# Kernel optimization log

Measured on AMD Instinct MI355X. Metric: run time of the kernel, lower is better.

Reference implementation:

```python
import jax, jax.numpy as jnp
import numpy as np

B, N, DIN, D, PHI, RHO, L = 4096, 10, 32, 128, 256, 128, 3
EPS = 1e-5


def setup_inputs() -> dict:
    key = jax.random.key(0)
    ks = jax.random.split(key, 24)
    def p(k, shape):
        return jax.random.normal(k, shape, jnp.float32) * 0.05
    return {
        "A": jax.random.normal(ks[0], (B, N, N), jnp.float32),
        "X": jax.random.normal(ks[1], (B, N, DIN), jnp.float32),
        "home_mask": jax.random.randint(ks[2], (B, N), 0, 2).astype(jnp.int32),
        "We1": p(ks[3], (DIN, D)), "be1": p(ks[4], (D,)),
        "We2": p(ks[5], (D, D)), "be2": p(ks[6], (D,)),
        "rgcn_w": p(ks[7], (L, 2, D, D)),      # per-relation weights
        "rgcn_root": p(ks[8], (L, D, D)),       # root (self) weight
        "rgcn_b": p(ks[9], (L, D)),
        "l1w": p(ks[10], (L, D, D)), "l1b": p(ks[11], (L, D)),
        "l2w": p(ks[12], (L, D, D)), "l2b": p(ks[13], (L, D)),
        "ln_g": jnp.ones((D,), jnp.float32), "ln_b": jnp.zeros((D,), jnp.float32),
        "p1w": p(ks[14], (D, PHI)), "p1b": p(ks[15], (PHI,)),
        "p2w": p(ks[16], (PHI, PHI)), "p2b": p(ks[17], (PHI,)),
        "r1w": p(ks[18], (PHI, RHO)), "r1b": p(ks[19], (RHO,)),
        "r2w": p(ks[20], (RHO, 1)), "r2b": p(ks[21], (1,)),
    }


def _layernorm(x, g, b):
    mu = x.mean(-1, keepdims=True)
    var = ((x - mu) ** 2).mean(-1, keepdims=True)
    return (x - mu) / jnp.sqrt(var + EPS) * g + b


def reference(A, X, home_mask, We1, be1, We2, be2, rgcn_w, rgcn_root, rgcn_b,
              l1w, l1b, l2w, l2b, ln_g, ln_b, p1w, p1b, p2w, p2b,
              r1w, r1b, r2w, r2b):
    BN = B * N
    hm = home_mask.astype(jnp.float32)
    am = 1.0 - hm
    # embedders (dropout layers are identity in eval)
    H = jax.nn.relu(X @ We1 + be1)
    H = (H @ We2 + be2).reshape(BN, D)
    # A ~ randn is nonzero everywhere -> edge list = all (b,i,j) pairs,
    # in the same row-major order torch.nonzero produces.
    bidx = jnp.repeat(jnp.arange(BN), N)          # b*N+i for each edge (row)
    row = bidx
    col = (jnp.repeat(jnp.arange(B), N * N) * N + jnp.tile(jnp.arange(N), BN))
    ew = A.reshape(-1)                             # edge weight
    aw = jnp.abs(ew)
    m1 = (ew > 0).astype(jnp.float32)              # relation 1 mask
    m0 = 1.0 - m1                                  # relation 0 mask
    agg = jnp.zeros_like(H)
    for l in range(L):
        H = H + agg
        # RGCNConv (mean aggregation per relation + root + bias)
        xj = H[row]                                # [E, D] gather of sources
        s0 = jax.ops.segment_sum(xj * m0[:, None], col, num_segments=BN)
        s1 = jax.ops.segment_sum(xj * m1[:, None], col, num_segments=BN)
        c0 = jax.ops.segment_sum(m0, col, num_segments=BN)
        c1 = jax.ops.segment_sum(m1, col, num_segments=BN)
        mean0 = s0 / jnp.maximum(c0, 1.0)[:, None]
        mean1 = s1 / jnp.maximum(c1, 1.0)[:, None]
        H2 = mean0 @ rgcn_w[l, 0] + mean1 @ rgcn_w[l, 1] + H @ rgcn_root[l] + rgcn_b[l]
        # outer gather-scale-scatter
        msg = H2[col] * aw[:, None]                # [E, D]
        agg = jax.ops.segment_sum(msg, row, num_segments=BN)
        agg = jax.nn.relu(_layernorm(agg, ln_g, ln_b))
        # Linear -> ReLU -> (Dropout=id) -> Linear
        agg = jax.nn.relu(agg @ l1w[l] + l1b[l])
        agg = agg @ l2w[l] + l2b[l]
    H = (H + agg).reshape(B, N, D)
    # DeepSet phi (dropout = identity)
    phi = jax.nn.relu(H @ p1w + p1b)
    phi = jax.nn.relu(phi @ p2w + p2b)             # [B, N, PHI]
    hs = (phi * hm[..., None]).sum(axis=1)
    aws = (phi * am[..., None]).sum(axis=1)
    def rho(s):
        return (jax.nn.relu(s @ r1w + r1b) @ r2w + r2b)[..., 0]
    return 0.5 + 0.5 * jnp.tanh(rho(hs) - rho(aws))
```

## Files before the change

### kernel.cpp

```cpp
#include <hip/hip_runtime.h>
#include <math.h>

#define B_    4096
#define N_    10
#define DIN_  32
#define D_    128
#define PHI_  256
#define RHO_  128
#define L_    3
#define EPS_  1e-5f

__device__ __forceinline__ short f2hs(float f) {
    union { _Float16 h; short s; } u;
    u.h = (_Float16)f;
    return u.s;
}
__device__ __forceinline__ float hs2f(short s) {
    union { _Float16 h; short s; } u;
    u.s = s;
    return (float)u.h;
}

typedef short    s16x8 __attribute__((ext_vector_type(8)));
typedef _Float16 h16x8 __attribute__((ext_vector_type(8)));
typedef float    f32x4 __attribute__((ext_vector_type(4)));
typedef float    v2f   __attribute__((ext_vector_type(2)));

__device__ __forceinline__ h16x8 ld8h(const short* p) {
    union { s16x8 s; h16x8 h; } u;
    u.s = *(const s16x8*)p;
    return u.h;
}
__device__ __forceinline__ h16x8 cvt8(const float* p) {
    f32x4 x0 = *(const f32x4*)p;
    f32x4 x1 = *(const f32x4*)(p + 4);
    h16x8 a;
    a[0]=(_Float16)x0[0]; a[1]=(_Float16)x0[1]; a[2]=(_Float16)x0[2]; a[3]=(_Float16)x0[3];
    a[4]=(_Float16)x1[0]; a[5]=(_Float16)x1[1]; a[6]=(_Float16)x1[2]; a[7]=(_Float16)x1[3];
    return a;
}

__device__ __forceinline__ v2f splat2(float s) { v2f r; r.x = s; r.y = s; return r; }
__device__ __forceinline__ v2f fma2(v2f a, v2f b, v2f c) { return __builtin_elementwise_fma(a, b, c); }

#define WS_WE1 0
#define WS_WE2 4096
#define WS_RGW 20480
#define WS_RGR 118784
#define WS_L1  167936
#define WS_L2  217088
#define WS_P1  266240
#define WS_P2  299008
#define WS_R1  364544

__global__ __launch_bounds__(256)
void prep_weights(const float* __restrict__ We1, const float* __restrict__ We2,
                  const float* __restrict__ rgw, const float* __restrict__ rgr,
                  const float* __restrict__ l1w, const float* __restrict__ l2w,
                  const float* __restrict__ p1w, const float* __restrict__ p2w,
                  const float* __restrict__ r1w, short* __restrict__ ws)
{
    int bi = blockIdx.x * 4 + (threadIdx.x >> 6);
    int l  = threadIdx.x & 63;
    const float* src; int KS, Nw, dstOff, tt;
    if      (bi <   8) { src = We1; KS = 1; Nw = 128; dstOff = WS_WE1; tt = bi; }
    else if (bi <  40) { src = We2; KS = 4; Nw = 128; dstOff = WS_WE2; tt = bi - 8; }
    else if (bi < 232) { int m = (bi - 40) >> 5;  src = rgw + m * 16384; KS = 4; Nw = 128; dstOff = WS_RGW + m * 16384; tt = (bi - 40)  & 31; }
    else if (bi < 328) { int m = (bi - 232) >> 5; src = rgr + m * 16384; KS = 4; Nw = 128; dstOff = WS_RGR + m * 16384; tt = (bi - 232) & 31; }
    else if (bi < 424) { int m = (bi - 328) >> 5; src = l1w + m * 16384; KS = 4; Nw = 128; dstOff = WS_L1  + m * 16384; tt = (bi - 328) & 31; }
    else if (bi < 520) { int m = (bi - 424) >> 5; src = l2w + m * 16384; KS = 4; Nw = 128; dstOff = WS_L2  + m * 16384; tt = (bi - 424) & 31; }
    else if (bi < 584) { src = p1w; KS = 4; Nw = 256; dstOff = WS_P1; tt = bi - 520; }
    else if (bi < 712) { src = p2w; KS = 8; Nw = 256; dstOff = WS_P2; tt = bi - 584; }
    else               { src = r1w; KS = 8; Nw = 128; dstOff = WS_R1; tt = bi - 712; }
    int nt = tt / KS, ks = tt - nt * KS;
    int kbase = ks * 32 + (l >> 4) * 8;
    int col   = nt * 16 + (l & 15);
    union { short s[8]; int4 v; } u;
#pragma unroll
    for (int j = 0; j < 8; ++j)
        u.s[j] = f2hs(src[(size_t)(kbase + j) * Nw + col]);
    *(int4*)(ws + dstOff + ((size_t)tt * 64 + l) * 8) = u.v;
}


#define MFMA16(a, b, c) __builtin_amdgcn_mfma_f32_16x16x32_f16(a, b, c, 0, 0, 0)

struct A4 { f32x4 p, q, r, s; };

__device__ __forceinline__ A4 a4init(const float* __restrict__ bias, int c16) {
    float b0 = bias[c16], b1 = bias[16 + c16];
    A4 c;
    c.p = (f32x4){b0, b0, b0, b0};
    c.q = (f32x4){b1, b1, b1, b1};
    c.r = c.p;
    c.s = c.q;
    return c;
}
__device__ __forceinline__ A4 a4zero() {
    A4 c;
    c.p = (f32x4){0.f, 0.f, 0.f, 0.f};
    c.q = c.p; c.r = c.p; c.s = c.p;
    return c;
}

template<int KS>
__device__ __forceinline__ A4 mm2q_a16(const short* __restrict__ Wf,
                                       const short* __restrict__ A0, const short* __restrict__ A1,
                                       int ldA, int mrow, int q, int l, A4 c) {
    static_assert(KS % 4 == 0, "KS must be a multiple of 4");
    const short* ap0 = A0 + mrow * ldA + q * 8;
    const short* ap1 = A1 + mrow * ldA + q * 8;
    const short* wp  = Wf + (size_t)l * 8;
#pragma unroll
    for (int kc = 0; kc < KS; kc += 4) {
        h16x8 fa0[4], fa1[4], fb0[4], fb1[4];
#pragma unroll
        for (int k = 0; k < 4; ++k) {
            fa0[k] = ld8h(ap0 + (kc + k) * 32);
            fa1[k] = ld8h(ap1 + (kc + k) * 32);
            fb0[k] = ld8h(wp + (size_t)(kc + k) * 512);
            fb1[k] = ld8h(wp + (size_t)(KS + kc + k) * 512);
        }
#pragma unroll
        for (int k = 0; k < 4; ++k) {
            c.p = MFMA16(fa0[k], fb0[k], c.p);
            c.r = MFMA16(fa1[k], fb0[k], c.r);
            c.q = MFMA16(fa0[k], fb1[k], c.q);
            c.s = MFMA16(fa1[k], fb1[k], c.s);
        }
    }
    return c;
}

template<int KS>
__device__ __forceinline__ A4 mm2q_a32(const short* __restrict__ Wf,
                                       const float* __restrict__ A0, const float* __restrict__ A1,
                                       int ldA, int mrow, int q, int l, A4 c) {
    static_assert(KS % 4 == 0, "KS must be a multiple of 4");
    const float* ap0 = A0 + mrow * ldA + q * 8;
    const float* ap1 = A1 + mrow * ldA + q * 8;
    const short* wp  = Wf + (size_t)l * 8;
#pragma unroll
    for (int kc = 0; kc < KS; kc += 4) {
        h16x8 fa0[4], fa1[4], fb0[4], fb1[4];
#pragma unroll
        for (int k = 0; k < 4; ++k) {
            fa0[k] = cvt8(ap0 + (kc + k) * 32);
            fa1[k] = cvt8(ap1 + (kc + k) * 32);
            fb0[k] = ld8h(wp + (size_t)(kc + k) * 512);
            fb1[k] = ld8h(wp + (size_t)(KS + kc + k) * 512);
        }
#pragma unroll
        for (int k = 0; k < 4; ++k) {
            c.p = MFMA16(fa0[k], fb0[k], c.p);
            c.r = MFMA16(fa1[k], fb0[k], c.r);
            c.q = MFMA16(fa0[k], fb1[k], c.q);
            c.s = MFMA16(fa1[k], fb1[k], c.s);
        }
    }
    return c;
}

#define HLD 132
#define SLD 392

template<bool RELU>
__device__ __forceinline__ void st2(f32x4 u, f32x4 v, short* __restrict__ dst, int q, int c16) {
#pragma unroll
    for (int i = 0; i < 4; ++i) {
        int r = q * 4 + i;
        if (r < 10) {
            float a = u[i], b = v[i];
            if (RELU) { a = fmaxf(a, 0.f); b = fmaxf(b, 0.f); }
            dst[r * SLD + c16]      = f2hs(a);
            dst[r * SLD + 16 + c16] = f2hs(b);
        }
    }
}

__device__ __forceinline__ void colsum1(f32x4 v4, const float* __restrict__ hmf,
                                        const float* __restrict__ awf,
                                        short* __restrict__ rho, int tt, int q, int c16, int l) {
    float v0 = fmaxf(v4[0], 0.f), v1 = fmaxf(v4[1], 0.f);
    float v2 = fmaxf(v4[2], 0.f), v3 = fmaxf(v4[3], 0.f);
    float hp = hmf[q * 4 + 0] * v0 + hmf[q * 4 + 1] * v1 + hmf[q * 4 + 2] * v2 + hmf[q * 4 + 3] * v3;
    float ap = awf[q * 4 + 0] * v0 + awf[q * 4 + 1] * v1 + awf[q * 4 + 2] * v2 + awf[q * 4 + 3] * v3;
    hp += __shfl_xor(hp, 16); hp += __shfl_xor(hp, 32);
    ap += __shfl_xor(ap, 16); ap += __shfl_xor(ap, 32);
    if (l < 16) {
        rho[tt * 16 + l]       = f2hs(hp);
        rho[256 + tt * 16 + l] = f2hs(ap);
    }
}

__device__ __forceinline__ void rhoepi1(f32x4 t0, f32x4 t1, const float* __restrict__ r2w,
                                        int wv, int q, int c16, int l, float* __restrict__ dSg) {
    float d = 0.f;
    if (q == 0) {
        d = (fmaxf(t0[0], 0.f) - fmaxf(t0[1], 0.f)) * r2w[(wv * 2 + 0) * 16 + c16];
        d = fmaf(fmaxf(t1[0], 0.f) - fmaxf(t1[1], 0.f), r2w[(wv * 2 + 1) * 16 + c16], d);
    }
#pragma unroll
    for (int off = 32; off > 0; off >>= 1) d += __shfl_xor(d, off);
    if (l == 0) dSg[wv] = d;
}

__global__ __attribute__((amdgpu_waves_per_eu(2, 5))) __launch_bounds__(256)
void gcn_main(const float* __restrict__ A, const float* __restrict__ X,
              const int* __restrict__ home_mask,
              const float* __restrict__ be1, const float* __restrict__ be2,
              const float* __restrict__ rgcn_b,
              const float* __restrict__ l1b, const float* __restrict__ l2b,
              const float* __restrict__ ln_g, const float* __restrict__ ln_b,
              const float* __restrict__ p1b, const float* __restrict__ p2b,
              const float* __restrict__ r1b, const float* __restrict__ r2w,
              const short* __restrict__ ws, float* __restrict__ out)
{
    const int b   = blockIdx.x;
    const int tid = threadIdx.x;
    const int wv  = tid >> 6;
    const int l   = tid & 63;
    const int q   = l >> 4;
    const int c16 = l & 15;
    const int mrow = (c16 < 10) ? c16 : 9;

    __shared__ __align__(16) float HfS[2][N_ * HLD];
    __shared__ __align__(16) short StS[2][N_ * SLD];
    __shared__ __align__(16) short RhoS[2][512];
    __shared__ float AsS[2][100];
    __shared__ float C0S[2][100], C1S[2][100];
    __shared__ float invc0S[2][N_], invc1S[2][N_], rsAS[2][N_];
    __shared__ float hmfS[2][16], awfS[2][16];
    __shared__ float dS[8];

    if (tid < 200) {
        int g = tid / 100, e = tid - g * 100;
        AsS[g][e] = A[(size_t)(2 * b + g) * 100 + e];
    }
    if (tid < 32) {
        int g = tid >> 4, idx = tid & 15;
        float hm = 0.f, aw = 0.f;
        if (idx < 10) { hm = (float)home_mask[(2 * b + g) * N_ + idx]; aw = 1.f - hm; }
        hmfS[g][idx] = hm; awfS[g][idx] = aw;
    }
    {
        A4 c = a4init(be1 + wv * 32, c16);
        h16x8 a0 = cvt8(X + (size_t)(2 * b + 0) * (N_ * DIN_) + mrow * DIN_ + q * 8);
        h16x8 a1 = cvt8(X + (size_t)(2 * b + 1) * (N_ * DIN_) + mrow * DIN_ + q * 8);
        h16x8 b0 = ld8h(ws + WS_WE1 + ((size_t)(wv * 2 + 0) * 64 + l) * 8);
        h16x8 b1 = ld8h(ws + WS_WE1 + ((size_t)(wv * 2 + 1) * 64 + l) * 8);
        c.p = MFMA16(a0, b0, c.p);
        c.r = MFMA16(a1, b0, c.r);
        c.q = MFMA16(a0, b1, c.q);
        c.s = MFMA16(a1, b1, c.s);
        st2<true>(c.p, c.q, StS[0] + wv * 32, q, c16);
        st2<true>(c.r, c.s, StS[1] + wv * 32, q, c16);
    }
    __syncthreads();

    if (tid < 20) {
        int g = tid / 10, j = tid - g * 10;
        float c1 = 0.f;
#pragma unroll
        for (int i = 0; i < 10; ++i) c1 += (AsS[g][i * 10 + j] > 0.f) ? 1.f : 0.f;
        invc1S[g][j] = 1.f / fmaxf(c1, 1.f);
        invc0S[g][j] = 1.f / fmaxf(10.f - c1, 1.f);
        float r = 0.f;
#pragma unroll
        for (int k = 0; k < 10; ++k) r += fabsf(AsS[g][j * 10 + k]);
        rsAS[g][j] = r;
    }
    {
        A4 c = a4init(be2 + wv * 32, c16);
        c = mm2q_a16<4>(ws + WS_WE2 + (size_t)wv * 4096, StS[0], StS[1], SLD, mrow, q, l, c);
#pragma unroll
        for (int i = 0; i < 4; ++i) {
            int r = q * 4 + i;
            if (r < 10) {
                HfS[0][r * HLD + wv * 32 + c16]      = c.p[i];
                HfS[0][r * HLD + wv * 32 + 16 + c16] = c.q[i];
                HfS[1][r * HLD + wv * 32 + c16]      = c.r[i];
                HfS[1][r * HLD + wv * 32 + 16 + c16] = c.s[i];
            }
        }
    }
    __syncthreads();

    if (tid < 200) {
        int g = tid / 100, e = tid - g * 100;
        int i = e / 10, k = e - i * 10;
        const float* As = AsS[g];
        float c0 = 0.f, c1 = 0.f;
#pragma unroll
        for (int j = 0; j < 10; ++j) {
            float aij = fabsf(As[i * 10 + j]);
            if (As[k * 10 + j] > 0.f) c1 += aij * invc1S[g][j];
            else                      c0 += aij * invc0S[g][j];
        }
        C0S[g][e] = c0; C1S[g][e] = c1;
    }
    __syncthreads();

    const v2f lg2 = *(const v2f*)(ln_g + 2 * l);
    const v2f lb2 = *(const v2f*)(ln_b + 2 * l);

    for (int ll = 0; ll < L_; ++ll) {
#pragma unroll 1
        for (int m = 0; m < 3; ++m) {
            const short* Wf;
            if      (m == 0) Wf = ws + WS_RGW + (size_t)(ll * 2 + 0) * 16384 + (size_t)wv * 4096;
            else if (m == 1) Wf = ws + WS_RGW + (size_t)(ll * 2 + 1) * 16384 + (size_t)wv * 4096;
            else             Wf = ws + WS_RGR + (size_t)ll * 16384 + (size_t)wv * 4096;
            A4 c = a4zero();
            c = mm2q_a32<4>(Wf, HfS[0], HfS[1], HLD, mrow, q, l, c);
            st2<false>(c.p, c.q, StS[0] + m * 128 + wv * 32, q, c16);
            st2<false>(c.r, c.s, StS[1] + m * 128 + wv * 32, q, c16);
        }
        __syncthreads();
        {
            v2f rb2 = *(const v2f*)(rgcn_b + ll * D_ + 2 * l);
            auto lnTask = [&](int t) -> short2 {
                int g = (t >= 10) ? 1 : 0, i = t - g * 10;
                const short* St = StS[g];
                const float* C0 = C0S[g] + i * 10;
                const float* C1 = C1S[g] + i * 10;
                const float* As = AsS[g] + i * 10;
                v2f ag = splat2(rsAS[g][i]) * rb2;
#pragma unroll
                for (int j = 0; j < 10; ++j) {
                    short2 h0 = *(const short2*)(St + j * SLD + 2 * l);
                    short2 h1 = *(const short2*)(St + j * SLD + 128 + 2 * l);
                    short2 hr = *(const short2*)(St + j * SLD + 256 + 2 * l);
                    v2f v0; v0.x = hs2f(h0.x); v0.y = hs2f(h0.y);
                    v2f v1; v1.x = hs2f(h1.x); v1.y = hs2f(h1.y);
                    v2f vr; vr.x = hs2f(hr.x); vr.y = hs2f(hr.y);
                    ag = fma2(splat2(C0[j]), v0, ag);
                    ag = fma2(splat2(C1[j]), v1, ag);
                    ag = fma2(splat2(fabsf(As[j])), vr, ag);
                }
                float sm = ag.x + ag.y;
                float ss = fmaf(ag.x, ag.x, ag.y * ag.y);
#pragma unroll
                for (int off = 32; off > 0; off >>= 1) {
                    sm += __shfl_xor(sm, off);
                    ss += __shfl_xor(ss, off);
                }
                float mu   = sm * (1.f / 128.f);
                float var  = ss * (1.f / 128.f) - mu * mu;
                float rstd = rsqrtf(var + EPS_);
                v2f v = fma2((ag - splat2(mu)) * splat2(rstd), lg2, lb2);
                short2 o;
                o.x = f2hs(fmaxf(v.x, 0.f));
                o.y = f2hs(fmaxf(v.y, 0.f));
                return o;
            };
            short2 ln0 = lnTask(wv);
            short2 ln1 = lnTask(wv + 4);
            short2 ln2 = lnTask(wv + 8);
            short2 ln3 = lnTask(wv + 12);
            short2 ln4 = lnTask(wv + 16);
            __syncthreads();
            auto stTask = [&](int t, short2 v) {
                int g = (t >= 10) ? 1 : 0, i = t - g * 10;
                *(short2*)(StS[g] + i * SLD + 2 * l) = v;
            };
            stTask(wv, ln0);
            stTask(wv + 4, ln1);
            stTask(wv + 8, ln2);
            stTask(wv + 12, ln3);
            stTask(wv + 16, ln4);
        }
        __syncthreads();
        {
            A4 c = a4init(l1b + ll * D_ + wv * 32, c16);
            c = mm2q_a16<4>(ws + WS_L1 + (size_t)ll * 16384 + (size_t)wv * 4096,
                            StS[0], StS[1], SLD, mrow, q, l, c);
            st2<true>(c.p, c.q, StS[0] + 128 + wv * 32, q, c16);
            st2<true>(c.r, c.s, StS[1] + 128 + wv * 32, q, c16);
        }
        __syncthreads();
        {
            A4 c = a4init(l2b + ll * D_ + wv * 32, c16);
            c = mm2q_a16<4>(ws + WS_L2 + (size_t)ll * 16384 + (size_t)wv * 4096,
                            StS[0] + 128, StS[1] + 128, SLD, mrow, q, l, c);
#pragma unroll
            for (int i = 0; i < 4; ++i) {
                int r = q * 4 + i;
                if (r < 10) {
                    HfS[0][r * HLD + wv * 32 + c16]      += c.p[i];
                    HfS[0][r * HLD + wv * 32 + 16 + c16] += c.q[i];
                    HfS[1][r * HLD + wv * 32 + c16]      += c.r[i];
                    HfS[1][r * HLD + wv * 32 + 16 + c16] += c.s[i];
                }
            }
        }
        __syncthreads();
    }

#pragma unroll 1
    for (int half = 0; half < 2; ++half) {
        const int nt0 = 4 * wv + 2 * half;
        A4 c = a4init(p1b + nt0 * 16, c16);
        c = mm2q_a32<4>(ws + WS_P1 + (size_t)nt0 * 2048, HfS[0], HfS[1], HLD, mrow, q, l, c);
        st2<true>(c.p, c.q, StS[0] + nt0 * 16, q, c16);
        st2<true>(c.r, c.s, StS[1] + nt0 * 16, q, c16);
    }
    __syncthreads();
#pragma unroll 1
    for (int half = 0; half < 2; ++half) {
        const int nt0 = 4 * wv + 2 * half;
        A4 c = a4init(p2b + nt0 * 16, c16);
        c = mm2q_a16<8>(ws + WS_P2 + (size_t)nt0 * 4096, StS[0], StS[1], SLD, mrow, q, l, c);
        colsum1(c.p, hmfS[0], awfS[0], RhoS[0], nt0,     q, c16, l);
        colsum1(c.q, hmfS[0], awfS[0], RhoS[0], nt0 + 1, q, c16, l);
        colsum1(c.r, hmfS[1], awfS[1], RhoS[1], nt0,     q, c16, l);
        colsum1(c.s, hmfS[1], awfS[1], RhoS[1], nt0 + 1, q, c16, l);
    }
    __syncthreads();
    {
        A4 c = a4init(r1b + wv * 32, c16);
        const int rr = (c16 < 2) ? c16 : 0;
        c = mm2q_a16<8>(ws + WS_R1 + (size_t)wv * 8192, RhoS[0], RhoS[1], 256, rr, q, l, c);
        rhoepi1(c.p, c.q, r2w, wv, q, c16, l, dS);
        rhoepi1(c.r, c.s, r2w, wv, q, c16, l, dS + 4);
    }
    __syncthreads();
    if (tid < 2)
        out[2 * b + tid] = 0.5f + 0.5f * tanhf(dS[tid * 4] + dS[tid * 4 + 1] +
                                               dS[tid * 4 + 2] + dS[tid * 4 + 3]);
}

extern "C" void kernel_launch(void* const* d_in, const int* in_sizes, int n_in,
                              void* d_out, int out_size, void* d_ws, size_t ws_size,
                              hipStream_t stream) {
    const float* A         = (const float*)d_in[0];
    const float* X         = (const float*)d_in[1];
    const int*   home_mask = (const int*)  d_in[2];
    const float* We1       = (const float*)d_in[3];
    const float* be1       = (const float*)d_in[4];
    const float* We2       = (const float*)d_in[5];
    const float* be2       = (const float*)d_in[6];
    const float* rgcn_w    = (const float*)d_in[7];
    const float* rgcn_root = (const float*)d_in[8];
    const float* rgcn_b    = (const float*)d_in[9];
    const float* l1w       = (const float*)d_in[10];
    const float* l1b       = (const float*)d_in[11];
    const float* l2w       = (const float*)d_in[12];
    const float* l2b       = (const float*)d_in[13];
    const float* ln_g      = (const float*)d_in[14];
    const float* ln_b      = (const float*)d_in[15];
    const float* p1w       = (const float*)d_in[16];
    const float* p1b       = (const float*)d_in[17];
    const float* p2w       = (const float*)d_in[18];
    const float* p2b       = (const float*)d_in[19];
    const float* r1w       = (const float*)d_in[20];
    const float* r1b       = (const float*)d_in[21];
    const float* r2w       = (const float*)d_in[22];

    short* ws = (short*)d_ws;

    prep_weights<<<194, 256, 0, stream>>>(We1, We2, rgcn_w, rgcn_root,
                                          l1w, l2w, p1w, p2w, r1w, ws);
    gcn_main<<<B_ / 2, 256, 0, stream>>>(A, X, home_mask, be1, be2, rgcn_b,
                                         l1b, l2b, ln_g, ln_b, p1b, p2b,
                                         r1b, r2w, ws, (float*)d_out);
}
```

Before: 240.5 us.

## Keep fp16 shadow of H in LDS and batch layernorm aggregation across groups

Adds a half-precision copy of the hidden state in shared memory, maintained alongside the fp32 copy. MFMA operand loads then read fp16 directly instead of loading fp32 and converting on every matmul. The layernorm aggregation is restructured so each wave handles rows from both graphs at once, reusing the loaded StS values across two graphs. Per-edge coefficients are kept in registers and broadcast with readlane instead of being read from LDS. The waves_per_eu cap is lowered from 5 to 4, which raises register pressure and adds extra LDS stores for the fp16 shadow.

```diff
diff --git a/kernel.cpp b/kernel.cpp
--- a/kernel.cpp
+++ b/kernel.cpp
@@ -42,6 +42,13 @@
 
 __device__ __forceinline__ v2f splat2(float s) { v2f r; r.x = s; r.y = s; return r; }
 __device__ __forceinline__ v2f fma2(v2f a, v2f b, v2f c) { return __builtin_elementwise_fma(a, b, c); }
+__device__ __forceinline__ v2f ld2f(const short* p) {
+    short2 h = *(const short2*)p;
+    v2f v; v.x = hs2f(h.x); v.y = hs2f(h.y); return v;
+}
+__device__ __forceinline__ float rdlane(float x, int lane) {
+    return __uint_as_float(__builtin_amdgcn_readlane(__float_as_uint(x), lane));
+}
 
 #define WS_WE1 0
 #define WS_WE2 4096
@@ -132,36 +139,8 @@
     return c;
 }
 
-template<int KS>
-__device__ __forceinline__ A4 mm2q_a32(const short* __restrict__ Wf,
-                                       const float* __restrict__ A0, const float* __restrict__ A1,
-                                       int ldA, int mrow, int q, int l, A4 c) {
-    static_assert(KS % 4 == 0, "KS must be a multiple of 4");
-    const float* ap0 = A0 + mrow * ldA + q * 8;
-    const float* ap1 = A1 + mrow * ldA + q * 8;
-    const short* wp  = Wf + (size_t)l * 8;
-#pragma unroll
-    for (int kc = 0; kc < KS; kc += 4) {
-        h16x8 fa0[4], fa1[4], fb0[4], fb1[4];
-#pragma unroll
-        for (int k = 0; k < 4; ++k) {
-            fa0[k] = cvt8(ap0 + (kc + k) * 32);
-            fa1[k] = cvt8(ap1 + (kc + k) * 32);
-            fb0[k] = ld8h(wp + (size_t)(kc + k) * 512);
-            fb1[k] = ld8h(wp + (size_t)(KS + kc + k) * 512);
-        }
-#pragma unroll
-        for (int k = 0; k < 4; ++k) {
-            c.p = MFMA16(fa0[k], fb0[k], c.p);
-            c.r = MFMA16(fa1[k], fb0[k], c.r);
-            c.q = MFMA16(fa0[k], fb1[k], c.q);
-            c.s = MFMA16(fa1[k], fb1[k], c.s);
-        }
-    }
-    return c;
-}
-
 #define HLD 132
+#define HH  136
 #define SLD 392
 
 template<bool RELU>
@@ -176,6 +155,24 @@
             dst[r * SLD + 16 + c16] = f2hs(b);
         }
     }
+}
+
+__device__ __forceinline__ short2 lnnorm(v2f ag, v2f lg2, v2f lb2) {
+    float sm = ag.x + ag.y;
+    float ss = fmaf(ag.x, ag.x, ag.y * ag.y);
+#pragma unroll
+    for (int off = 32; off > 0; off >>= 1) {
+        sm += __shfl_xor(sm, off);
+        ss += __shfl_xor(ss, off);
+    }
+    float mu   = sm * (1.f / 128.f);
+    float var  = ss * (1.f / 128.f) - mu * mu;
+    float rstd = rsqrtf(var + EPS_);
+    v2f v = fma2((ag - splat2(mu)) * splat2(rstd), lg2, lb2);
+    short2 o;
+    o.x = f2hs(fmaxf(v.x, 0.f));
+    o.y = f2hs(fmaxf(v.y, 0.f));
+    return o;
 }
 
 __device__ __forceinline__ void colsum1(f32x4 v4, const float* __restrict__ hmf,
@@ -205,7 +202,7 @@
     if (l == 0) dSg[wv] = d;
 }
 
-__global__ __attribute__((amdgpu_waves_per_eu(2, 5))) __launch_bounds__(256)
+__global__ __attribute__((amdgpu_waves_per_eu(2, 4))) __launch_bounds__(256)
 void gcn_main(const float* __restrict__ A, const float* __restrict__ X,
               const int* __restrict__ home_mask,
               const float* __restrict__ be1, const float* __restrict__ be2,
@@ -225,6 +222,7 @@
     const int mrow = (c16 < 10) ? c16 : 9;
 
     __shared__ __align__(16) float HfS[2][N_ * HLD];
+    __shared__ __align__(16) short HhS[2][N_ * HH];
     __shared__ __align__(16) short StS[2][N_ * SLD];
     __shared__ __align__(16) short RhoS[2][512];
     __shared__ float AsS[2][100];
@@ -281,6 +279,10 @@
                 HfS[0][r * HLD + wv * 32 + 16 + c16] = c.q[i];
                 HfS[1][r * HLD + wv * 32 + c16]      = c.r[i];
                 HfS[1][r * HLD + wv * 32 + 16 + c16] = c.s[i];
+                HhS[0][r * HH + wv * 32 + c16]       = f2hs(c.p[i]);
+                HhS[0][r * HH + wv * 32 + 16 + c16]  = f2hs(c.q[i]);
+                HhS[1][r * HH + wv * 32 + c16]       = f2hs(c.r[i]);
+                HhS[1][r * HH + wv * 32 + 16 + c16]  = f2hs(c.s[i]);
             }
         }
     }
@@ -300,6 +302,20 @@
         C0S[g][e] = c0; C1S[g][e] = c1;
     }
     __syncthreads();
+
+    float cf0 = 0.f, cf1 = 0.f, cfa = 0.f, cfr = 0.f;
+    {
+        int jj = l / 6, rem = l - jj * 6;
+        int dd = rem >> 1, gg = rem & 1;
+        int ri = wv + 4 * dd;
+        if (l < 60 && ri < 10) {
+            cf0 = C0S[gg][ri * 10 + jj];
+            cf1 = C1S[gg][ri * 10 + jj];
+            cfa = fabsf(AsS[gg][ri * 10 + jj]);
+        }
+        int dd2 = l >> 1, gg2 = l & 1, ri2 = wv + 4 * dd2;
+        if (l < 6 && ri2 < 10) cfr = rsAS[gg2][ri2];
+    }
 
     const v2f lg2 = *(const v2f*)(ln_g + 2 * l);
     const v2f lb2 = *(const v2f*)(ln_b + 2 * l);
@@ -312,63 +328,65 @@
             else if (m == 1) Wf = ws + WS_RGW + (size_t)(ll * 2 + 1) * 16384 + (size_t)wv * 4096;
             else             Wf = ws + WS_RGR + (size_t)ll * 16384 + (size_t)wv * 4096;
             A4 c = a4zero();
-            c = mm2q_a32<4>(Wf, HfS[0], HfS[1], HLD, mrow, q, l, c);
+            c = mm2q_a16<4>(Wf, HhS[0], HhS[1], HH, mrow, q, l, c);
             st2<false>(c.p, c.q, StS[0] + m * 128 + wv * 32, q, c16);
             st2<false>(c.r, c.s, StS[1] + m * 128 + wv * 32, q, c16);
         }
         __syncthreads();
         {
             v2f rb2 = *(const v2f*)(rgcn_b + ll * D_ + 2 * l);
-            auto lnTask = [&](int t) -> short2 {
-                int g = (t >= 10) ? 1 : 0, i = t - g * 10;
-                const short* St = StS[g];
-                const float* C0 = C0S[g] + i * 10;
-                const float* C1 = C1S[g] + i * 10;
-                const float* As = AsS[g] + i * 10;
-                v2f ag = splat2(rsAS[g][i]) * rb2;
-#pragma unroll
-                for (int j = 0; j < 10; ++j) {
-                    short2 h0 = *(const short2*)(St + j * SLD + 2 * l);
-                    short2 h1 = *(const short2*)(St + j * SLD + 128 + 2 * l);
-                    short2 hr = *(const short2*)(St + j * SLD + 256 + 2 * l);
-                    v2f v0; v0.x = hs2f(h0.x); v0.y = hs2f(h0.y);
-                    v2f v1; v1.x = hs2f(h1.x); v1.y = hs2f(h1.y);
-                    v2f vr; vr.x = hs2f(hr.x); vr.y = hs2f(hr.y);
-                    ag = fma2(splat2(C0[j]), v0, ag);
-                    ag = fma2(splat2(C1[j]), v1, ag);
-                    ag = fma2(splat2(fabsf(As[j])), vr, ag);
-                }
-                float sm = ag.x + ag.y;
-                float ss = fmaf(ag.x, ag.x, ag.y * ag.y);
-#pragma unroll
-                for (int off = 32; off > 0; off >>= 1) {
-                    sm += __shfl_xor(sm, off);
-                    ss += __shfl_xor(ss, off);
-                }
-                float mu   = sm * (1.f / 128.f);
-                float var  = ss * (1.f / 128.f) - mu * mu;
-                float rstd = rsqrtf(var + EPS_);
-                v2f v = fma2((ag - splat2(mu)) * splat2(rstd), lg2, lb2);
-                short2 o;
-                o.x = f2hs(fmaxf(v.x, 0.f));
-                o.y = f2hs(fmaxf(v.y, 0.f));
-                return o;
-            };
-            short2 ln0 = lnTask(wv);
-            short2 ln1 = lnTask(wv + 4);
-            short2 ln2 = lnTask(wv + 8);
-            short2 ln3 = lnTask(wv + 12);
-            short2 ln4 = lnTask(wv + 16);
+            v2f ag00 = splat2(rdlane(cfr, 0)) * rb2;
+            v2f ag01 = splat2(rdlane(cfr, 1)) * rb2;
+            v2f ag10 = splat2(rdlane(cfr, 2)) * rb2;
+            v2f ag11 = splat2(rdlane(cfr, 3)) * rb2;
+            v2f ag20 = splat2(rdlane(cfr, 4)) * rb2;
+            v2f ag21 = splat2(rdlane(cfr, 5)) * rb2;
+#pragma unroll
+            for (int j = 0; j < 10; ++j) {
+                const short* pa = StS[0] + j * SLD + 2 * l;
+                const short* pb = StS[1] + j * SLD + 2 * l;
+                v2f va0 = ld2f(pa), va1 = ld2f(pa + 128), var_ = ld2f(pa + 256);
+                v2f vb0 = ld2f(pb), vb1 = ld2f(pb + 128), vbr  = ld2f(pb + 256);
+                ag00 = fma2(splat2(rdlane(cf0, j * 6 + 0)), va0, ag00);
+                ag00 = fma2(splat2(rdlane(cf1, j * 6 + 0)), va1, ag00);
+                ag00 = fma2(splat2(rdlane(cfa, j * 6 + 0)), var_, ag00);
+                ag01 = fma2(splat2(rdlane(cf0, j * 6 + 1)), vb0, ag01);
+                ag01 = fma2(splat2(rdlane(cf1, j * 6 + 1)), vb1, ag01);
+                ag01 = fma2(splat2(rdlane(cfa, j * 6 + 1)), vbr, ag01);
+                ag10 = fma2(splat2(rdlane(cf0, j * 6 + 2)), va0, ag10);
+                ag10 = fma2(splat2(rdlane(cf1, j * 6 + 2)), va1, ag10);
+                ag10 = fma2(splat2(rdlane(cfa, j * 6 + 2)), var_, ag10);
+                ag11 = fma2(splat2(rdlane(cf0, j * 6 + 3)), vb0, ag11);
+                ag11 = fma2(splat2(rdlane(cf1, j * 6 + 3)), vb1, ag11);
+                ag11 = fma2(splat2(rdlane(cfa, j * 6 + 3)), vbr, ag11);
+                ag20 = fma2(splat2(rdlane(cf0, j * 6 + 4)), va0, ag20);
+                ag20 = fma2(splat2(rdlane(cf1, j * 6 + 4)), va1, ag20);
+                ag20 = fma2(splat2(rdlane(cfa, j * 6 + 4)), var_, ag20);
+                ag21 = fma2(splat2(rdlane(cf0, j * 6 + 5)), vb0, ag21);
+                ag21 = fma2(splat2(rdlane(cf1, j * 6 + 5)), vb1, ag21);
+                ag21 = fma2(splat2(rdlane(cfa, j * 6 + 5)), vbr, ag21);
+            }
+            const int r2i = wv + 8;
+            const bool v2ok = (r2i < 10);
+            short2 o00 = lnnorm(ag00, lg2, lb2);
+            short2 o01 = lnnorm(ag01, lg2, lb2);
+            short2 o10 = lnnorm(ag10, lg2, lb2);
+            short2 o11 = lnnorm(ag11, lg2, lb2);
+            short2 o20, o21;
+            o20.x = o20.y = o21.x = o21.y = 0;
+            if (v2ok) {
+                o20 = lnnorm(ag20, lg2, lb2);
+                o21 = lnnorm(ag21, lg2, lb2);
+            }
             __syncthreads();
-            auto stTask = [&](int t, short2 v) {
-                int g = (t >= 10) ? 1 : 0, i = t - g * 10;
-                *(short2*)(StS[g] + i * SLD + 2 * l) = v;
-            };
-            stTask(wv, ln0);
-            stTask(wv + 4, ln1);
-            stTask(wv + 8, ln2);
-            stTask(wv + 12, ln3);
-            stTask(wv + 16, ln4);
+            *(short2*)(StS[0] + wv * SLD + 2 * l)       = o00;
+            *(short2*)(StS[1] + wv * SLD + 2 * l)       = o01;
+            *(short2*)(StS[0] + (wv + 4) * SLD + 2 * l) = o10;
+            *(short2*)(StS[1] + (wv + 4) * SLD + 2 * l) = o11;
+            if (v2ok) {
+                *(short2*)(StS[0] + r2i * SLD + 2 * l)  = o20;
+                *(short2*)(StS[1] + r2i * SLD + 2 * l)  = o21;
+            }
         }
         __syncthreads();
         {
@@ -387,10 +405,18 @@
             for (int i = 0; i < 4; ++i) {
                 int r = q * 4 + i;
                 if (r < 10) {
-                    HfS[0][r * HLD + wv * 32 + c16]      += c.p[i];
-                    HfS[0][r * HLD + wv * 32 + 16 + c16] += c.q[i];
-                    HfS[1][r * HLD + wv * 32 + c16]      += c.r[i];
-                    HfS[1][r * HLD + wv * 32 + 16 + c16] += c.s[i];
+                    float n0 = HfS[0][r * HLD + wv * 32 + c16]      + c.p[i];
+                    float n1 = HfS[0][r * HLD + wv * 32 + 16 + c16] + c.q[i];
+                    float n2 = HfS[1][r * HLD + wv * 32 + c16]      + c.r[i];
+                    float n3 = HfS[1][r * HLD + wv * 32 + 16 + c16] + c.s[i];
+                    HfS[0][r * HLD + wv * 32 + c16]      = n0;
+                    HfS[0][r * HLD + wv * 32 + 16 + c16] = n1;
+                    HfS[1][r * HLD + wv * 32 + c16]      = n2;
+                    HfS[1][r * HLD + wv * 32 + 16 + c16] = n3;
+                    HhS[0][r * HH + wv * 32 + c16]       = f2hs(n0);
+                    HhS[0][r * HH + wv * 32 + 16 + c16]  = f2hs(n1);
+                    HhS[1][r * HH + wv * 32 + c16]       = f2hs(n2);
+                    HhS[1][r * HH + wv * 32 + 16 + c16]  = f2hs(n3);
                 }
             }
         }
@@ -401,7 +427,7 @@
     for (int half = 0; half < 2; ++half) {
         const int nt0 = 4 * wv + 2 * half;
         A4 c = a4init(p1b + nt0 * 16, c16);
-        c = mm2q_a32<4>(ws + WS_P1 + (size_t)nt0 * 2048, HfS[0], HfS[1], HLD, mrow, q, l, c);
+        c = mm2q_a16<4>(ws + WS_P1 + (size_t)nt0 * 2048, HhS[0], HhS[1], HH, mrow, q, l, c);
         st2<true>(c.p, c.q, StS[0] + nt0 * 16, q, c16);
         st2<true>(c.r, c.s, StS[1] + nt0 * 16, q, c16);
     }
```

New measurement: 253.9 us. 5.5% more time.
